# Optimization experiments

Hardware: AMD Instinct MI355X
Metric: run time of the kernel (lower is better)

The kernel has to match this reference:

```python
import jax, jax.numpy as jnp
import numpy as np
from jax import lax


def _edit_distance(ow, tg):
    # ow: [B, S] int predicted words; tg: [B, T] int targets
    B, S = ow.shape
    T = tg.shape[1]
    f32 = jnp.float32
    row0 = jnp.broadcast_to(jnp.arange(T + 1, dtype=f32), (B, T + 1))  # dp[:,0,:] = j

    def outer(prev_row, oi):  # prev_row: [B, T+1], oi: [B] = output_words[:, i-1]
        mask = (oi[:, None] == tg).astype(f32)          # [B, T]
        up = prev_row[:, 1:]                            # dp[:, i-1, j]
        diag = prev_row[:, :-1]                         # dp[:, i-1, j-1]
        first = prev_row[:, 0] + 1.0                    # dp[:, i, 0] = i

        def inner(left, xs):  # left: [B] = dp[:, i, j-1]
            u, d, m = xs
            new = m * d + (1.0 - m) * (jnp.minimum(jnp.minimum(u, left), d) + 1.0)
            return new, new

        _, rowvals = lax.scan(inner, first, (up.T, diag.T, mask.T))  # [T, B]
        new_row = jnp.concatenate([first[:, None], rowvals.T], axis=1)
        return new_row, None

    final_row, _ = lax.scan(outer, row0, ow.T)  # scan over i = 1..S
    return final_row[:, -1]  # dp[:, S, T]


def setup_inputs() -> dict:
    key = jax.random.key(0)
    k1, k2 = jax.random.split(key)
    output = jax.random.normal(k1, (16, 512, 32000), dtype=jnp.float32)
    target = jax.random.randint(k2, (16, 512), 0, 32000, dtype=jnp.int32)
    return {"output": output, "target": target}


def reference(output, target):
    # softmax does not change argmax but is kept for faithfulness to the original
    probs = jax.nn.softmax(output, axis=-1)
    output_words = jnp.argmax(probs, axis=-1).astype(jnp.int32)  # [B, S]
    dist = _edit_distance(output_words, target)                   # [B]
    T = target.shape[1]
    return jnp.mean(dist / jnp.float32(T))
```

## Files before the change

kernel.cpp:

```cpp
#include <hip/hip_runtime.h>
#include <math.h>

#define VOCAB 32000
#define BATCH 16
#define SEQ   512
#define RPL   8

typedef float floatx4 __attribute__((ext_vector_type(4)));

__global__ __launch_bounds__(256) void argmax_kernel(const float* __restrict__ logits,
                                                     int* __restrict__ words,
                                                     float* __restrict__ out) {
    if (blockIdx.x == 0 && threadIdx.x == 0) out[0] = 0.0f;

    const int wid  = threadIdx.x >> 6;
    const int lane = threadIdx.x & 63;
    const int row  = blockIdx.x * 4 + wid;
    const floatx4* base4 = (const floatx4*)(logits + (size_t)row * VOCAB);

    float best = -INFINITY;
    int bestIdx = 0x7FFFFFFF;

    #pragma unroll 5
    for (int k = lane; k < VOCAB / 4; k += 64) {
        floatx4 v = __builtin_nontemporal_load(base4 + k);
        int i0 = k * 4;
        if (v.x > best) { best = v.x; bestIdx = i0;     }
        if (v.y > best) { best = v.y; bestIdx = i0 + 1; }
        if (v.z > best) { best = v.z; bestIdx = i0 + 2; }
        if (v.w > best) { best = v.w; bestIdx = i0 + 3; }
    }

    for (int off = 32; off > 0; off >>= 1) {
        float ov = __shfl_down(best, off, 64);
        int   oi = __shfl_down(bestIdx, off, 64);
        if (ov > best || (ov == best && oi < bestIdx)) { best = ov; bestIdx = oi; }
    }
    if (lane == 0) words[row] = bestIdx;
}

__global__ __launch_bounds__(64) void editdist_kernel(const int* __restrict__ words,
                                                      const int* __restrict__ target,
                                                      float* __restrict__ out) {
    const int b = blockIdx.x;
    const int t = threadIdx.x;

    __shared__ int s_tg[SEQ];
    #pragma unroll
    for (int k = 0; k < RPL; ++k)
        s_tg[t + 64 * k] = target[b * SEQ + t + 64 * k];
    __syncthreads();

    int myw[RPL];
    #pragma unroll
    for (int r = 0; r < RPL; ++r)
        myw[r] = words[b * SEQ + t * RPL + r];

    int colv[RPL];
    #pragma unroll
    for (int r = 0; r < RPL; ++r) colv[r] = t * RPL + 1 + r;
    int prev_up = t * RPL;

    const int NSTEP = SEQ + 63;
    for (int s = 1; s <= NSTEP; ++s) {
        int up_in = __shfl_up(colv[RPL - 1], 1, 64);
        const int j = s - t;
        if (t == 0) up_in = s;
        if (j >= 1 && j <= SEQ) {
            const int tgj = s_tg[j - 1];
            int mp[RPL];
            mp[0] = min(colv[0], prev_up - (myw[0] == tgj ? 1 : 0)) + 1;
            #pragma unroll
            for (int r = 1; r < RPL; ++r)
                mp[r] = min(colv[r], colv[r - 1] - (myw[r] == tgj ? 1 : 0)) + 1;
            int u = up_in;
            #pragma unroll
            for (int r = 0; r < RPL; ++r) {
                u = min(u + 1, mp[r]);
                colv[r] = u;
            }
            prev_up = up_in;
        }
    }

    if (t == 63)
        atomicAdd(out, (float)colv[RPL - 1] * (1.0f / ((float)BATCH * (float)SEQ)));
}

extern "C" void kernel_launch(void* const* d_in, const int* in_sizes, int n_in,
                              void* d_out, int out_size, void* d_ws, size_t ws_size,
                              hipStream_t stream) {
    const float* logits = (const float*)d_in[0];
    const int*   target = (const int*)d_in[1];

    int* words = (int*)d_ws;
    float* out = (float*)d_out;

    argmax_kernel<<<BATCH * SEQ / 4, 256, 0, stream>>>(logits, words, out);
    editdist_kernel<<<BATCH, 64, 0, stream>>>(words, target, out);
}
```

Before: 253.3 us.

## Fuse argmax and edit-distance into one kernel with flag-based streaming overlap

Merges the argmax and edit-distance kernels into one launch. Sixteen blocks run the wavefront DP and spin-wait on per-word ready flags (word index + 1), while the other blocks compute argmax rows in sequence-major order and publish them with relaxed atomics. The DP swaps roles so targets sit in registers and predicted words stream along the anti-diagonal through shuffles. This lets the serial DP overlap the memory-bound argmax pass. In exchange it adds an init kernel, relies on the DP blocks being resident alongside the producer blocks, and risks spinning or stalling if they are not.

```diff
diff --git a/kernel.cpp b/kernel.cpp
--- a/kernel.cpp
+++ b/kernel.cpp
@@ -5,86 +5,121 @@
 #define BATCH 16
 #define SEQ   512
 #define RPL   8
+#define NED   16
+#define NAMX  1024
 
 typedef float floatx4 __attribute__((ext_vector_type(4)));
 
-__global__ __launch_bounds__(256) void argmax_kernel(const float* __restrict__ logits,
-                                                     int* __restrict__ words,
-                                                     float* __restrict__ out) {
-    if (blockIdx.x == 0 && threadIdx.x == 0) out[0] = 0.0f;
+__global__ void init_kernel(int* __restrict__ words, float* __restrict__ out) {
+    int g = blockIdx.x * 256 + threadIdx.x;
+    if (g < BATCH * SEQ) words[g] = 0;
+    if (g == 0) out[0] = 0.0f;
+}
 
+__global__ __launch_bounds__(256) void fused_kernel(const float* __restrict__ logits,
+                                                    const int* __restrict__ target,
+                                                    int* __restrict__ words,
+                                                    float* __restrict__ out) {
     const int wid  = threadIdx.x >> 6;
     const int lane = threadIdx.x & 63;
-    const int row  = blockIdx.x * 4 + wid;
-    const floatx4* base4 = (const floatx4*)(logits + (size_t)row * VOCAB);
 
-    float best = -INFINITY;
-    int bestIdx = 0x7FFFFFFF;
+    if (blockIdx.x < NED) {
+        if (wid != 0) return;
+        const int b = blockIdx.x;
+        const int t = lane;
 
-    #pragma unroll 5
-    for (int k = lane; k < VOCAB / 4; k += 64) {
-        floatx4 v = __builtin_nontemporal_load(base4 + k);
-        int i0 = k * 4;
-        if (v.x > best) { best = v.x; bestIdx = i0;     }
-        if (v.y > best) { best = v.y; bestIdx = i0 + 1; }
-        if (v.z > best) { best = v.z; bestIdx = i0 + 2; }
-        if (v.w > best) { best = v.w; bestIdx = i0 + 3; }
+        int myt[RPL];
+        #pragma unroll
+        for (int r = 0; r < RPL; ++r)
+            myt[r] = target[b * SEQ + t * RPL + r] + 1;
+
+        int colv[RPL];
+        #pragma unroll
+        for (int r = 0; r < RPL; ++r) colv[r] = t * RPL + 1 + r;
+        int prev_up = t * RPL;
+
+        const int* wptr = words + b * SEQ;
+        int p0 = 0, p1 = 0;
+        if (t == 0) {
+            p0 = __hip_atomic_load(&wptr[0], __ATOMIC_RELAXED, __HIP_MEMORY_SCOPE_AGENT);
+            p1 = __hip_atomic_load(&wptr[1], __ATOMIC_RELAXED, __HIP_MEMORY_SCOPE_AGENT);
+        }
+
+        int w_prev = 0;
+        const int NSTEP = SEQ + 63;
+        for (int s = 1; s <= NSTEP; ++s) {
+            int w_this = __shfl_up(w_prev, 1, 64);
+            if (t == 0) {
+                if (s <= SEQ) {
+                    while (p0 == 0) {
+                        __builtin_amdgcn_s_sleep(2);
+                        p0 = __hip_atomic_load(&wptr[s - 1], __ATOMIC_RELAXED,
+                                               __HIP_MEMORY_SCOPE_AGENT);
+                    }
+                    w_this = p0;
+                    p0 = p1;
+                    p1 = (s + 1 <= SEQ)
+                       ? __hip_atomic_load(&wptr[s + 1], __ATOMIC_RELAXED,
+                                           __HIP_MEMORY_SCOPE_AGENT)
+                       : 0;
+                }
+            }
+
+            int up_in = __shfl_up(colv[RPL - 1], 1, 64);
+            if (t == 0) up_in = s;
+
+            const int j = s - t;
+            if (j >= 1 && j <= SEQ) {
+                int mp[RPL];
+                mp[0] = min(colv[0], prev_up - (myt[0] == w_this ? 1 : 0)) + 1;
+                #pragma unroll
+                for (int r = 1; r < RPL; ++r)
+                    mp[r] = min(colv[r], colv[r - 1] - (myt[r] == w_this ? 1 : 0)) + 1;
+                int u = up_in;
+                #pragma unroll
+                for (int r = 0; r < RPL; ++r) {
+                    u = min(u + 1, mp[r]);
+                    colv[r] = u;
+                }
+                prev_up = up_in;
+            }
+            w_prev = w_this;
+        }
+
+        if (t == 63)
+            atomicAdd(out, (float)colv[RPL - 1] * (1.0f / ((float)BATCH * (float)SEQ)));
+        return;
     }
 
-    for (int off = 32; off > 0; off >>= 1) {
-        float ov = __shfl_down(best, off, 64);
-        int   oi = __shfl_down(bestIdx, off, 64);
-        if (ov > best || (ov == best && oi < bestIdx)) { best = ov; bestIdx = oi; }
+    const int wgid = (blockIdx.x - NED) * 4 + wid;
+    #pragma unroll
+    for (int k = 0; k < 2; ++k) {
+        const int l   = k * 4096 + wgid;
+        const int row = (l & 15) * SEQ + (l >> 4);
+        const floatx4* base4 = (const floatx4*)(logits + (size_t)row * VOCAB);
+
+        float best = -INFINITY;
+        int bestIdx = 0x7FFFFFFF;
+
+        #pragma unroll 5
+        for (int kk = lane; kk < VOCAB / 4; kk += 64) {
+            floatx4 v = __builtin_nontemporal_load(base4 + kk);
+            int i0 = kk * 4;
+            if (v.x > best) { best = v.x; bestIdx = i0;     }
+            if (v.y > best) { best = v.y; bestIdx = i0 + 1; }
+            if (v.z > best) { best = v.z; bestIdx = i0 + 2; }
+            if (v.w > best) { best = v.w; bestIdx = i0 + 3; }
+        }
+
+        for (int off = 32; off > 0; off >>= 1) {
+            float ov = __shfl_down(best, off, 64);
+            int   oi = __shfl_down(bestIdx, off, 64);
+            if (ov > best || (ov == best && oi < bestIdx)) { best = ov; bestIdx = oi; }
+        }
+        if (lane == 0)
+            __hip_atomic_store(&words[row], bestIdx + 1, __ATOMIC_RELAXED,
+                               __HIP_MEMORY_SCOPE_AGENT);
     }
-    if (lane == 0) words[row] = bestIdx;
-}
-
-__global__ __launch_bounds__(64) void editdist_kernel(const int* __restrict__ words,
-                                                      const int* __restrict__ target,
-                                                      float* __restrict__ out) {
-    const int b = blockIdx.x;
-    const int t = threadIdx.x;
-
-    __shared__ int s_tg[SEQ];
-    #pragma unroll
-    for (int k = 0; k < RPL; ++k)
-        s_tg[t + 64 * k] = target[b * SEQ + t + 64 * k];
-    __syncthreads();
-
-    int myw[RPL];
-    #pragma unroll
-    for (int r = 0; r < RPL; ++r)
-        myw[r] = words[b * SEQ + t * RPL + r];
-
-    int colv[RPL];
-    #pragma unroll
-    for (int r = 0; r < RPL; ++r) colv[r] = t * RPL + 1 + r;
-    int prev_up = t * RPL;
-
-    const int NSTEP = SEQ + 63;
-    for (int s = 1; s <= NSTEP; ++s) {
-        int up_in = __shfl_up(colv[RPL - 1], 1, 64);
-        const int j = s - t;
-        if (t == 0) up_in = s;
-        if (j >= 1 && j <= SEQ) {
-            const int tgj = s_tg[j - 1];
-            int mp[RPL];
-            mp[0] = min(colv[0], prev_up - (myw[0] == tgj ? 1 : 0)) + 1;
-            #pragma unroll
-            for (int r = 1; r < RPL; ++r)
-                mp[r] = min(colv[r], colv[r - 1] - (myw[r] == tgj ? 1 : 0)) + 1;
-            int u = up_in;
-            #pragma unroll
-            for (int r = 0; r < RPL; ++r) {
-                u = min(u + 1, mp[r]);
-                colv[r] = u;
-            }
-            prev_up = up_in;
-        }
-    }
-
-    if (t == 63)
-        atomicAdd(out, (float)colv[RPL - 1] * (1.0f / ((float)BATCH * (float)SEQ)));
 }
 
 extern "C" void kernel_launch(void* const* d_in, const int* in_sizes, int n_in,
@@ -96,6 +131,6 @@
     int* words = (int*)d_ws;
     float* out = (float*)d_out;
 
-    argmax_kernel<<<BATCH * SEQ / 4, 256, 0, stream>>>(logits, words, out);
-    editdist_kernel<<<BATCH, 64, 0, stream>>>(words, target, out);
+    init_kernel<<<(BATCH * SEQ + 255) / 256, 256, 0, stream>>>(words, out);
+    fused_kernel<<<NED + NAMX, 256, 0, stream>>>(logits, target, words, out);
 }
```

Measured after the change: 308.8 us. 1.22x slower.
